# Optimization experiments

Measured on AMD Instinct MI355X. Metric: run time of the kernel, lower is better.

The kernel has to match this reference:

```python
import jax, jax.numpy as jnp
import numpy as np

DIM = 768
NH = 12
HD = DIM // NH
MLP = 4 * DIM
EPS = 1e-5


def _ln(x, w, b):
    mu = x.mean(-1, keepdims=True)
    var = ((x - mu) ** 2).mean(-1, keepdims=True)
    return (x - mu) * jax.lax.rsqrt(var + EPS) * w + b


def setup_inputs() -> dict:
    key = jax.random.key(0)
    ks = jax.random.split(key, 12)
    s = 0.02
    return {
        "xq": jax.random.normal(ks[0], (4, 32, 32, DIM), jnp.float32),
        "xkv": jax.random.normal(ks[1], (4, 64, 64, DIM), jnp.float32),
        "norm1_w": jnp.ones((DIM,), jnp.float32),
        "norm1_b": jnp.zeros((DIM,), jnp.float32),
        "kv_w": jax.random.normal(ks[2], (DIM, 2 * DIM), jnp.float32) * s,
        "kv_b": jnp.zeros((2 * DIM,), jnp.float32),
        "q_w": jax.random.normal(ks[3], (DIM, DIM), jnp.float32) * s,
        "q_b": jnp.zeros((DIM,), jnp.float32),
        "proj_w": jax.random.normal(ks[4], (DIM, DIM), jnp.float32) * s,
        "proj_b": jnp.zeros((DIM,), jnp.float32),
        "norm2_w": jnp.ones((DIM,), jnp.float32),
        "norm2_b": jnp.zeros((DIM,), jnp.float32),
        "mlp_w1": jax.random.normal(ks[5], (DIM, MLP), jnp.float32) * s,
        "mlp_b1": jnp.zeros((MLP,), jnp.float32),
        "mlp_w2": jax.random.normal(ks[6], (MLP, DIM), jnp.float32) * s,
        "mlp_b2": jnp.zeros((DIM,), jnp.float32),
    }


def reference(xq, xkv, norm1_w, norm1_b, kv_w, kv_b, q_w, q_b, proj_w, proj_b,
              norm2_w, norm2_b, mlp_w1, mlp_b1, mlp_w2, mlp_b2):
    B, Hq, Wq, C = xq.shape
    _, H, W, _ = xkv.shape
    shortcut = xq
    xn = _ln(xq, norm1_w, norm1_b)
    # kv projection: [B, H*W, 2, NH, HD]
    kv = (xkv.reshape(B, H * W, C) @ kv_w + kv_b).reshape(B, H * W, 2, NH, HD)
    k = kv[:, :, 0].transpose(0, 2, 1, 3)  # [B, NH, HW, HD]
    v = kv[:, :, 1].transpose(0, 2, 1, 3)
    q = (xn.reshape(B, Hq * Wq, C) @ q_w + q_b).reshape(B, Hq * Wq, NH, HD).transpose(0, 2, 1, 3)
    scale = HD ** -0.5
    attn = jnp.einsum('bhqd,bhkd->bhqk', q * scale, k)
    attn = jax.nn.softmax(attn, axis=-1)
    o = jnp.einsum('bhqk,bhkd->bhqd', attn, v)  # [B, NH, HqWq, HD]
    o = o.transpose(0, 2, 1, 3).reshape(B, Hq, Wq, C)
    o = o @ proj_w + proj_b
    x = shortcut + o
    xn2 = _ln(x, norm2_w, norm2_b)
    mlp = jax.nn.gelu(xn2 @ mlp_w1 + mlp_b1, approximate=False) @ mlp_w2 + mlp_b2
    return x + mlp
```

## Files before the change

### kernel.cpp

```cpp
#include <hip/hip_runtime.h>
#include <hip/hip_bf16.h>
#include <math.h>

#define DIM 768
#define NH 12
#define HD 64
#define NQ 1024
#define NKV 4096
#define QSCALE 0.18033688011112042f

typedef __attribute__((ext_vector_type(4))) float f32x4;
typedef __attribute__((ext_vector_type(16))) float f32x16;
typedef __attribute__((ext_vector_type(8))) __bf16 bf16x8;
typedef __attribute__((ext_vector_type(8))) unsigned short u16x8;
typedef __attribute__((ext_vector_type(4))) unsigned short u16x4;
typedef unsigned short u16;

typedef const __attribute__((address_space(1))) void* gas_t;
typedef __attribute__((address_space(3))) void* las_t;

__device__ __forceinline__ void gl16(const void* g, void* l) {
    __builtin_amdgcn_global_load_lds((gas_t)g, (las_t)l, 16, 0, 0);
}

__device__ __forceinline__ u16 f2b(float x) {
    __bf16 h = (__bf16)x;
    return __builtin_bit_cast(u16, h);
}

__device__ __forceinline__ float b2f(u16 x) {
    unsigned int u = ((unsigned int)x) << 16;
    return __builtin_bit_cast(float, u);
}

__device__ __forceinline__ f32x4 mfma16(const u16* a, const u16* b, f32x4 c) {
    bf16x8 av = *reinterpret_cast<const bf16x8*>(a);
    bf16x8 bv = *reinterpret_cast<const bf16x8*>(b);
    return __builtin_amdgcn_mfma_f32_16x16x32_bf16(av, bv, c, 0, 0, 0);
}

__device__ __forceinline__ f32x16 mfma32(bf16x8 a, bf16x8 b, f32x16 c) {
    return __builtin_amdgcn_mfma_f32_32x32x16_bf16(a, b, c, 0, 0, 0);
}

__global__ __launch_bounds__(256) void cast_bf16_kernel(
    const float* __restrict__ in, u16* __restrict__ out, int n8)
{
    int i = blockIdx.x * 256 + threadIdx.x;
    if (i >= n8) return;
    const float4* p = reinterpret_cast<const float4*>(in) + (size_t)i * 2;
    float4 a = p[0], b = p[1];
    u16x8 o;
    o[0] = f2b(a.x); o[1] = f2b(a.y); o[2] = f2b(a.z); o[3] = f2b(a.w);
    o[4] = f2b(b.x); o[5] = f2b(b.y); o[6] = f2b(b.z); o[7] = f2b(b.w);
    reinterpret_cast<u16x8*>(out)[i] = o;
}

__global__ __launch_bounds__(256) void transpose_cast_kernel(
    const float* __restrict__ W, u16* __restrict__ Wt, int K, int N)
{
    __shared__ u16 T[64][72];
    int k0 = blockIdx.y * 64, n0 = blockIdx.x * 64;
    int tid = threadIdx.x;
    int r = tid >> 2, c = (tid & 3) * 16;
    const float* src = W + (size_t)(k0 + r) * N + n0 + c;
    #pragma unroll
    for (int j = 0; j < 16; j += 4) {
        float4 f = *reinterpret_cast<const float4*>(src + j);
        T[r][c + j + 0] = f2b(f.x); T[r][c + j + 1] = f2b(f.y);
        T[r][c + j + 2] = f2b(f.z); T[r][c + j + 3] = f2b(f.w);
    }
    __syncthreads();
    int d = tid >> 2, c2 = (tid & 3) * 16;
    u16x8 o0, o1;
    #pragma unroll
    for (int j = 0; j < 8; ++j) o0[j] = T[c2 + j][d];
    #pragma unroll
    for (int j = 0; j < 8; ++j) o1[j] = T[c2 + 8 + j][d];
    u16* dst = Wt + (size_t)(n0 + d) * K + k0 + c2;
    *reinterpret_cast<u16x8*>(dst) = o0;
    *reinterpret_cast<u16x8*>(dst + 8) = o1;
}

__global__ __launch_bounds__(256) void ln_kernel(
    const float* __restrict__ x, const float* __restrict__ w,
    const float* __restrict__ b, u16* __restrict__ out)
{
    int row = blockIdx.x;
    const float* xr = x + (size_t)row * DIM;
    int tid = threadIdx.x;
    float v0 = xr[tid], v1 = xr[tid + 256], v2 = xr[tid + 512];
    float s = v0 + v1 + v2;
    float s2 = v0 * v0 + v1 * v1 + v2 * v2;
    for (int off = 1; off < 64; off <<= 1) {
        s += __shfl_xor(s, off);
        s2 += __shfl_xor(s2, off);
    }
    __shared__ float ss[4], ss2[4];
    int wid = tid >> 6, lane = tid & 63;
    if (lane == 0) { ss[wid] = s; ss2[wid] = s2; }
    __syncthreads();
    s = ss[0] + ss[1] + ss[2] + ss[3];
    s2 = ss2[0] + ss2[1] + ss2[2] + ss2[3];
    float mu = s * (1.0f / DIM);
    float var = s2 * (1.0f / DIM) - mu * mu;
    float r = rsqrtf(var + 1e-5f);
    u16* orow = out + (size_t)row * DIM;
    orow[tid]       = f2b((v0 - mu) * r * w[tid]       + b[tid]);
    orow[tid + 256] = f2b((v1 - mu) * r * w[tid + 256] + b[tid + 256]);
    orow[tid + 512] = f2b((v2 - mu) * r * w[tid + 512] + b[tid + 512]);
}

template <int EPI>
__global__ __launch_bounds__(256) void gemm_kernel(
    const u16* __restrict__ A, const u16* __restrict__ Bt,
    const float* __restrict__ bias, const float* __restrict__ res,
    void* __restrict__ out, void* __restrict__ out2, int M, int N, int K)
{
    __shared__ u16 As[2][4096];
    __shared__ u16 Bs[2][4096];
    int p = blockIdx.x;
    int nbx = N >> 7;
    int ypx = (M >> 7) >> 3;
    int xcd = p & 7, slot = p >> 3;
    int by = xcd * ypx + slot / nbx;
    int bx = slot - (slot / nbx) * nbx;
    int n0 = bx * 128, m0 = by * 128;
    int tid = threadIdx.x, lane = tid & 63, wave = tid >> 6;
    int wm = (wave >> 1) * 64, wn = (wave & 1) * 64;
    f32x4 acc[4][4] = {};

    int ca = tid, cb = tid + 256;
    int ra = ca >> 2, sa = ((ca & 3) ^ (ra & 3)) * 8;
    int rb = cb >> 2, sb = ((cb & 3) ^ (rb & 3)) * 8;
    const u16* Asrc1 = A + (size_t)(m0 + ra) * K + sa;
    const u16* Asrc2 = A + (size_t)(m0 + rb) * K + sb;
    const u16* Bsrc1 = Bt + (size_t)(n0 + ra) * K + sa;
    const u16* Bsrc2 = Bt + (size_t)(n0 + rb) * K + sb;

    auto STAGE = [&](int buf, int k0) {
        gl16(Asrc1 + k0, &As[buf][ca * 8]);
        gl16(Asrc2 + k0, &As[buf][cb * 8]);
        gl16(Bsrc1 + k0, &Bs[buf][ca * 8]);
        gl16(Bsrc2 + k0, &Bs[buf][cb * 8]);
    };

    int fr = lane & 15, fq = lane >> 4;
    int co = (fq ^ (fr & 3)) * 8;

    auto COMPUTE = [&](int buf) {
        #pragma unroll
        for (int mf = 0; mf < 4; ++mf) {
            const u16* a = &As[buf][(wm + mf * 16 + fr) * 32 + co];
            #pragma unroll
            for (int nf = 0; nf < 4; ++nf)
                acc[mf][nf] = mfma16(a, &Bs[buf][(wn + nf * 16 + fr) * 32 + co],
                                     acc[mf][nf]);
        }
    };

    STAGE(0, 0);
    asm volatile("s_waitcnt vmcnt(0)" ::: "memory");
    __builtin_amdgcn_s_barrier();
    for (int k0 = 0; k0 < K; k0 += 64) {
        STAGE(1, k0 + 32);
        COMPUTE(0);
        asm volatile("s_waitcnt vmcnt(0)" ::: "memory");
        __builtin_amdgcn_s_barrier();
        if (k0 + 64 < K) STAGE(0, k0 + 64);
        COMPUTE(1);
        asm volatile("s_waitcnt vmcnt(0)" ::: "memory");
        __builtin_amdgcn_s_barrier();
    }

    if constexpr (EPI == 4) {
        u16* kb = reinterpret_cast<u16*>(out);
        u16* vtb = reinterpret_cast<u16*>(out2);
        if (n0 < 768) {
            #pragma unroll
            for (int mf = 0; mf < 4; ++mf)
                #pragma unroll
                for (int nf = 0; nf < 4; ++nf) {
                    int col = n0 + wn + nf * 16 + fr;
                    float bv = bias[col];
                    #pragma unroll
                    for (int r = 0; r < 4; ++r) {
                        int row = m0 + wm + mf * 16 + fq * 4 + r;
                        kb[(size_t)row * 768 + col] = f2b(acc[mf][nf][r] + bv);
                    }
                }
        } else {
            #pragma unroll
            for (int mf = 0; mf < 4; ++mf)
                #pragma unroll
                for (int nf = 0; nf < 4; ++nf) {
                    int col = n0 + wn + nf * 16 + fr;
                    int c = col - 768, h = c >> 6, d = c & 63;
                    float bv = bias[col];
                    int row0 = m0 + wm + mf * 16 + fq * 4;
                    int bb = row0 >> 12, kvi = row0 & 4095;
                    int kv6 = kvi & 63;
                    int slot = (kv6 & 51) | ((kv6 & 4) << 1) | ((kv6 & 8) >> 1);
                    u16x4 pv;
                    #pragma unroll
                    for (int r = 0; r < 4; ++r) pv[r] = f2b(acc[mf][nf][r] + bv);
                    *reinterpret_cast<u16x4*>(vtb + ((size_t)(bb * 12 + h) * 64 + d) * 4096
                                              + (kvi & ~63) + slot) = pv;
                }
        }
        return;
    }

    float* outf = reinterpret_cast<float*>(out);
    u16* outb = reinterpret_cast<u16*>(out);
    #pragma unroll
    for (int mf = 0; mf < 4; ++mf)
        #pragma unroll
        for (int nf = 0; nf < 4; ++nf)
            #pragma unroll
            for (int r = 0; r < 4; ++r) {
                int row = m0 + wm + mf * 16 + fq * 4 + r;
                int col = n0 + wn + nf * 16 + fr;
                size_t idx = (size_t)row * N + col;
                float v = acc[mf][nf][r] + bias[col];
                if constexpr (EPI == 2) {
                    outf[idx] = v + res[idx];
                } else {
                    float g = 0.5f * v * (1.0f + erff(v * 0.70710678118f));
                    outb[idx] = f2b(g);
                }
            }
}

template <int EPI>
__global__ __launch_bounds__(256) void gemm64_kernel(
    const u16* __restrict__ A, const u16* __restrict__ Bt,
    const float* __restrict__ bias, const float* __restrict__ res,
    void* __restrict__ out, int M, int N, int K)
{
    __shared__ u16 As[2][4096];
    __shared__ u16 Bs[2][4096];
    int p = blockIdx.x;
    int nbx = N >> 6;
    int ypx = (M >> 6) >> 3;
    int xcd = p & 7, slot = p >> 3;
    int by = xcd * ypx + slot / nbx;
    int bx = slot - (slot / nbx) * nbx;
    int n0 = bx * 64, m0 = by * 64;
    int tid = threadIdx.x, lane = tid & 63, wave = tid >> 6;
    int wm = (wave >> 1) * 32, wn = (wave & 1) * 32;
    f32x4 acc[2][2] = {};

    int c1 = tid, c2 = tid + 256;
    int r1 = c1 >> 3, s1 = ((c1 & 7) ^ (r1 & 7)) * 8;
    int r2 = c2 >> 3, s2 = ((c2 & 7) ^ (r2 & 7)) * 8;
    const u16* As1 = A + (size_t)(m0 + r1) * K + s1;
    const u16* As2 = A + (size_t)(m0 + r2) * K + s2;
    const u16* Bt1 = Bt + (size_t)(n0 + r1) * K + s1;
    const u16* Bt2 = Bt + (size_t)(n0 + r2) * K + s2;

    auto STAGE = [&](int buf, int k0) {
        gl16(As1 + k0, &As[buf][c1 * 8]);
        gl16(As2 + k0, &As[buf][c2 * 8]);
        gl16(Bt1 + k0, &Bs[buf][c1 * 8]);
        gl16(Bt2 + k0, &Bs[buf][c2 * 8]);
    };

    int fr = lane & 15, fq = lane >> 4;
    int co0 = (fq ^ (fr & 7)) * 8;
    int co1 = ((4 + fq) ^ (fr & 7)) * 8;

    STAGE(0, 0);
    asm volatile("s_waitcnt vmcnt(0)" ::: "memory");
    __builtin_amdgcn_s_barrier();
    int NIT = K >> 6;
    for (int it = 0; it < NIT; ++it) {
        int cur = it & 1;
        if (it + 1 < NIT) STAGE(cur ^ 1, (it + 1) << 6);
        #pragma unroll
        for (int mf = 0; mf < 2; ++mf) {
            const u16* arow = &As[cur][(wm + mf * 16 + fr) * 64];
            #pragma unroll
            for (int nf = 0; nf < 2; ++nf) {
                const u16* brow = &Bs[cur][(wn + nf * 16 + fr) * 64];
                acc[mf][nf] = mfma16(arow + co0, brow + co0, acc[mf][nf]);
                acc[mf][nf] = mfma16(arow + co1, brow + co1, acc[mf][nf]);
            }
        }
        asm volatile("s_waitcnt vmcnt(0)" ::: "memory");
        __builtin_amdgcn_s_barrier();
    }

    float* outf = reinterpret_cast<float*>(out);
    u16* outb = reinterpret_cast<u16*>(out);
    #pragma unroll
    for (int mf = 0; mf < 2; ++mf)
        #pragma unroll
        for (int nf = 0; nf < 2; ++nf)
            #pragma unroll
            for (int r = 0; r < 4; ++r) {
                int row = m0 + wm + mf * 16 + fq * 4 + r;
                int col = n0 + wn + nf * 16 + fr;
                size_t idx = (size_t)row * N + col;
                float v = acc[mf][nf][r] + bias[col];
                if constexpr (EPI == 1) {
                    outb[idx] = f2b(v * QSCALE);
                } else {
                    outf[idx] = v + res[idx];
                }
            }
}

__global__ __launch_bounds__(256, 4) void attn_kernel(
    const u16* __restrict__ q, const u16* __restrict__ kbuf,
    const u16* __restrict__ vt, u16* __restrict__ op0, u16* __restrict__ op1,
    float* __restrict__ L)
{
    int p = blockIdx.x;
    int xcd = p & 7, slot = p >> 3;
    int bh = xcd * 6 + (slot >> 5);
    int rem = slot & 31;
    int qt = rem >> 1, half = rem & 1;
    int h = bh % NH, bb = bh / NH;
    const int NIT = 32;

    __shared__ u16 Kb[2][4096];
    __shared__ u16 Vb[2][4096];
    __shared__ float lx[64];

    int tid = threadIdx.x, lane = tid & 63, wave = tid >> 6;
    int qb = wave >> 1, kh = wave & 1;
    int l31 = lane & 31, hi = lane >> 5;
    int sw = l31 & 7;

    u16x8 ov = {0x3F80, 0x3F80, 0x3F80, 0x3F80, 0x3F80, 0x3F80, 0x3F80, 0x3F80};
    const bf16x8 ONES = __builtin_bit_cast(bf16x8, ov);

    bf16x8 qf[4];
    {
        const u16* qbp = q + (size_t)(bb * NQ + qt * 64 + qb * 32 + l31) * DIM
                         + h * HD + hi * 8;
        #pragma unroll
        for (int ks = 0; ks < 4; ++ks)
            qf[ks] = *reinterpret_cast<const bf16x8*>(qbp + ks * 16);
    }

    int c1 = tid, c2 = tid + 256;
    int r1 = c1 >> 3, sc1 = (c1 & 7) ^ (r1 & 7);
    int r2 = c2 >> 3, sc2 = (c2 & 7) ^ (r2 & 7);
    size_t krow0 = (size_t)bb * NKV + half * 2048;
    const u16* ks1 = kbuf + (krow0 + r1) * 768 + h * HD + sc1 * 8;
    const u16* ks2 = kbuf + (krow0 + r2) * 768 + h * HD + sc2 * 8;
    const u16* vs1 = vt + ((size_t)bh * HD + r1) * NKV + half * 2048 + sc1 * 8;
    const u16* vs2 = vt + ((size_t)bh * HD + r2) * NKV + half * 2048 + sc2 * 8;

    auto STAGE = [&](int buf, int kv0) {
        gl16(ks1 + (size_t)kv0 * 768, &Kb[buf][c1 * 8]);
        gl16(ks2 + (size_t)kv0 * 768, &Kb[buf][c2 * 8]);
        gl16(vs1 + kv0, &Vb[buf][c1 * 8]);
        gl16(vs2 + kv0, &Vb[buf][c2 * 8]);
    };

    f32x16 oacc0 = {}, oacc1 = {}, lsum = {};

    STAGE(0, 0);
    asm volatile("s_waitcnt vmcnt(0)" ::: "memory");
    __builtin_amdgcn_s_barrier();

    int krow = kh * 32 + l31;
    const int kroff = krow * 64;
    int vc0 = ((kh * 4 + 0 * 2 + hi) ^ sw) * 8;
    int vc1 = ((kh * 4 + 1 * 2 + hi) ^ sw) * 8;
    int krsw = krow & 7;

    auto BODY = [&](int cur, int it) {
        if (it + 1 < NIT) STAGE(cur ^ 1, (it + 1) * 64);
        const u16* kb = &Kb[cur][kroff];
        const u16* vb = &Vb[cur][l31 * 64];
        f32x16 s = {};
        __builtin_amdgcn_s_setprio(1);
        #pragma unroll
        for (int ks = 0; ks < 4; ++ks) {
            bf16x8 kf = *reinterpret_cast<const bf16x8*>(
                kb + (((ks * 2 + hi) ^ krsw) * 8));
            s = mfma32(kf, qf[ks], s);
        }
        __builtin_amdgcn_s_setprio(0);
        u16x8 p0, p1;
        #pragma unroll
        for (int r = 0; r < 8; ++r) p0[r] = f2b(exp2f(s[r]));
        #pragma unroll
        for (int r = 0; r < 8; ++r) p1[r] = f2b(exp2f(s[r + 8]));
        bf16x8 a0 = __builtin_bit_cast(bf16x8, p0);
        bf16x8 a1 = __builtin_bit_cast(bf16x8, p1);
        __builtin_amdgcn_s_setprio(1);
        lsum = mfma32(a0, ONES, lsum);
        lsum = mfma32(a1, ONES, lsum);
        bf16x8 v00 = *reinterpret_cast<const bf16x8*>(vb + vc0);
        bf16x8 v01 = *reinterpret_cast<const bf16x8*>(vb + vc1);
        bf16x8 v10 = *reinterpret_cast<const bf16x8*>(vb + 2048 + vc0);
        bf16x8 v11 = *reinterpret_cast<const bf16x8*>(vb + 2048 + vc1);
        oacc0 = mfma32(a0, v00, oacc0);
        oacc0 = mfma32(a1, v01, oacc0);
        oacc1 = mfma32(a0, v10, oacc1);
        oacc1 = mfma32(a1, v11, oacc1);
        __builtin_amdgcn_s_setprio(0);
        asm volatile("s_waitcnt vmcnt(0)" ::: "memory");
        __builtin_amdgcn_s_barrier();
    };

    for (int it = 0; it < NIT; it += 2) { BODY(0, it); BODY(1, it + 1); }

    float* ox = reinterpret_cast<float*>(&Kb[0][0]);
    if (kh) {
        #pragma unroll
        for (int r = 0; r < 16; ++r) {
            int qrow = (r & 3) + 8 * (r >> 2) + 4 * hi;
            ox[(qb * 32 + qrow) * 64 + l31] = oacc0[r];
            ox[(qb * 32 + qrow) * 64 + 32 + l31] = oacc1[r];
        }
        if (l31 == 0) {
            #pragma unroll
            for (int r = 0; r < 16; ++r) {
                int qrow = (r & 3) + 8 * (r >> 2) + 4 * hi;
                lx[qb * 32 + qrow] = lsum[r];
            }
        }
    }
    __syncthreads();
    if (!kh) {
        u16* op = half ? op1 : op0;
        float lt[16];
        #pragma unroll
        for (int r = 0; r < 16; ++r) {
            int qrow = (r & 3) + 8 * (r >> 2) + 4 * hi;
            lt[r] = lsum[r] + lx[qb * 32 + qrow];
        }
        if (l31 == 0) {
            #pragma unroll
            for (int r = 0; r < 16; ++r) {
                int qrow = (r & 3) + 8 * (r >> 2) + 4 * hi;
                L[half * 49152 + bh * 1024 + qt * 64 + qb * 32 + qrow] = lt[r];
            }
        }
        #pragma unroll
        for (int r = 0; r < 16; ++r) {
            int qrow = (r & 3) + 8 * (r >> 2) + 4 * hi;
            float rcl = 1.0f / lt[r];
            float t0 = oacc0[r] + ox[(qb * 32 + qrow) * 64 + l31];
            float t1 = oacc1[r] + ox[(qb * 32 + qrow) * 64 + 32 + l31];
            size_t orow = (size_t)(bb * NQ + qt * 64 + qb * 32 + qrow) * DIM + h * HD;
            op[orow + l31] = f2b(t0 * rcl);
            op[orow + 32 + l31] = f2b(t1 * rcl);
        }
    }
}

__global__ __launch_bounds__(256) void combine_kernel(
    const u16* __restrict__ op0, const u16* __restrict__ op1,
    const float* __restrict__ L, u16* __restrict__ out)
{
    int idx = blockIdx.x * 256 + threadIdx.x;
    int t = idx / 96, cc = (idx - t * 96) * 8;
    int h = cc >> 6;
    int bb = t >> 10, qr = t & 1023;
    int li = (bb * 12 + h) * 1024 + qr;
    float l0 = L[li], l1 = L[49152 + li];
    float w0 = l0 / (l0 + l1), w1 = 1.0f - w0;
    u16x8 a = *reinterpret_cast<const u16x8*>(op0 + (size_t)t * 768 + cc);
    u16x8 b = *reinterpret_cast<const u16x8*>(op1 + (size_t)t * 768 + cc);
    u16x8 o;
    #pragma unroll
    for (int j = 0; j < 8; ++j) o[j] = f2b(b2f(a[j]) * w0 + b2f(b[j]) * w1);
    *reinterpret_cast<u16x8*>(out + (size_t)t * 768 + cc) = o;
}

extern "C" void kernel_launch(void* const* d_in, const int* in_sizes, int n_in,
                              void* d_out, int out_size, void* d_ws, size_t ws_size,
                              hipStream_t stream) {
    const float* xq  = (const float*)d_in[0];
    const float* xkv = (const float*)d_in[1];
    const float* n1w = (const float*)d_in[2];
    const float* n1b = (const float*)d_in[3];
    const float* kvw = (const float*)d_in[4];
    const float* kvb = (const float*)d_in[5];
    const float* qw  = (const float*)d_in[6];
    const float* qb  = (const float*)d_in[7];
    const float* pjw = (const float*)d_in[8];
    const float* pjb = (const float*)d_in[9];
    const float* n2w = (const float*)d_in[10];
    const float* n2b = (const float*)d_in[11];
    const float* w1  = (const float*)d_in[12];
    const float* b1  = (const float*)d_in[13];
    const float* w2  = (const float*)d_in[14];
    const float* b2  = (const float*)d_in[15];
    float* xout = (float*)d_out;

    char* ws = (char*)d_ws;
    u16* xkv_b  = (u16*)(ws);
    u16* kbuf   = (u16*)(ws + 25165824);
    u16* vt     = (u16*)(ws + 50331648);
    u16* xn_bf  = (u16*)(ws + 75497472);
    u16* q_bf   = (u16*)(ws + 81788928);
    u16* o_bf   = (u16*)(ws + 88080384);
    u16* wkv_bf = (u16*)(ws + 94371840);
    u16* wq_bf  = (u16*)(ws + 96731136);
    u16* wpj_bf = (u16*)(ws + 97910784);
    u16* w1_bf  = (u16*)(ws + 99090432);
    u16* w2_bf  = (u16*)(ws + 103809024);
    u16* hid    = xkv_b;
    float* Lbuf = (float*)wkv_bf;

    cast_bf16_kernel<<<dim3(6144), dim3(256), 0, stream>>>(xkv, xkv_b, 1572864);
    transpose_cast_kernel<<<dim3(24, 12), dim3(256), 0, stream>>>(kvw, wkv_bf, 768, 1536);
    transpose_cast_kernel<<<dim3(12, 12), dim3(256), 0, stream>>>(qw, wq_bf, 768, 768);
    transpose_cast_kernel<<<dim3(12, 12), dim3(256), 0, stream>>>(pjw, wpj_bf, 768, 768);
    transpose_cast_kernel<<<dim3(48, 12), dim3(256), 0, stream>>>(w1, w1_bf, 768, 3072);
    transpose_cast_kernel<<<dim3(12, 48), dim3(256), 0, stream>>>(w2, w2_bf, 3072, 768);

    ln_kernel<<<dim3(4096), dim3(256), 0, stream>>>(xq, n1w, n1b, xn_bf);
    gemm_kernel<4><<<dim3(12 * 128), dim3(256), 0, stream>>>(xkv_b, wkv_bf, kvb, nullptr, kbuf, vt, 16384, 1536, 768);
    gemm64_kernel<1><<<dim3(768), dim3(256), 0, stream>>>(xn_bf, wq_bf, qb, nullptr, q_bf, 4096, 768, 768);
    attn_kernel<<<dim3(1536), dim3(256), 0, stream>>>(q_bf, kbuf, vt, xn_bf, o_bf, Lbuf);
    combine_kernel<<<dim3(1536), dim3(256), 0, stream>>>(xn_bf, o_bf, Lbuf, q_bf);
    gemm64_kernel<2><<<dim3(768), dim3(256), 0, stream>>>(q_bf, wpj_bf, pjb, xq, xout, 4096, 768, 768);
    ln_kernel<<<dim3(4096), dim3(256), 0, stream>>>(xout, n2w, n2b, xn_bf);
    gemm_kernel<3><<<dim3(24 * 32), dim3(256), 0, stream>>>(xn_bf, w1_bf, b1, nullptr, hid, nullptr, 4096, 3072, 768);
    gemm64_kernel<2><<<dim3(768), dim3(256), 0, stream>>>(hid, w2_bf, b2, xout, xout, 4096, 768, 3072);
}
```

Baseline: 290.9 us.

## Split attention KV into quarters with 128-query tiles, dropping intra-block reduction

Each attention block now handles 128 queries (one 32-row query slab per wave) over a quarter of the KV sequence, with each wave iterating over both 32-key halves of every staged tile. Previously a block covered 64 queries over half the KV, and two waves per query slab split the keys, so their partial outputs had to be merged through LDS with a barrier. That LDS merge disappears and each staged K/V tile is reused by twice as many queries. The cost is four partial outputs instead of two, so the combine kernel reads and weights four bf16 buffers and L values, which adds global memory traffic.

```diff
diff --git a/kernel.cpp b/kernel.cpp
--- a/kernel.cpp
+++ b/kernel.cpp
@@ -314,22 +314,20 @@
 __global__ __launch_bounds__(256, 4) void attn_kernel(
     const u16* __restrict__ q, const u16* __restrict__ kbuf,
     const u16* __restrict__ vt, u16* __restrict__ op0, u16* __restrict__ op1,
-    float* __restrict__ L)
+    u16* __restrict__ op2, u16* __restrict__ op3, float* __restrict__ L)
 {
     int p = blockIdx.x;
     int xcd = p & 7, slot = p >> 3;
     int bh = xcd * 6 + (slot >> 5);
     int rem = slot & 31;
-    int qt = rem >> 1, half = rem & 1;
+    int qt = rem >> 2, quarter = rem & 3;
     int h = bh % NH, bb = bh / NH;
-    const int NIT = 32;
+    const int NIT = 16;
 
     __shared__ u16 Kb[2][4096];
     __shared__ u16 Vb[2][4096];
-    __shared__ float lx[64];
 
     int tid = threadIdx.x, lane = tid & 63, wave = tid >> 6;
-    int qb = wave >> 1, kh = wave & 1;
     int l31 = lane & 31, hi = lane >> 5;
     int sw = l31 & 7;
 
@@ -338,7 +336,7 @@
 
     bf16x8 qf[4];
     {
-        const u16* qbp = q + (size_t)(bb * NQ + qt * 64 + qb * 32 + l31) * DIM
+        const u16* qbp = q + (size_t)(bb * NQ + qt * 128 + wave * 32 + l31) * DIM
                          + h * HD + hi * 8;
         #pragma unroll
         for (int ks = 0; ks < 4; ++ks)
@@ -348,11 +346,11 @@
     int c1 = tid, c2 = tid + 256;
     int r1 = c1 >> 3, sc1 = (c1 & 7) ^ (r1 & 7);
     int r2 = c2 >> 3, sc2 = (c2 & 7) ^ (r2 & 7);
-    size_t krow0 = (size_t)bb * NKV + half * 2048;
+    size_t krow0 = (size_t)bb * NKV + quarter * 1024;
     const u16* ks1 = kbuf + (krow0 + r1) * 768 + h * HD + sc1 * 8;
     const u16* ks2 = kbuf + (krow0 + r2) * 768 + h * HD + sc2 * 8;
-    const u16* vs1 = vt + ((size_t)bh * HD + r1) * NKV + half * 2048 + sc1 * 8;
-    const u16* vs2 = vt + ((size_t)bh * HD + r2) * NKV + half * 2048 + sc2 * 8;
+    const u16* vs1 = vt + ((size_t)bh * HD + r1) * NKV + quarter * 1024 + sc1 * 8;
+    const u16* vs2 = vt + ((size_t)bh * HD + r2) * NKV + quarter * 1024 + sc2 * 8;
 
     auto STAGE = [&](int buf, int kv0) {
         gl16(ks1 + (size_t)kv0 * 768, &Kb[buf][c1 * 8]);
@@ -367,97 +365,70 @@
     asm volatile("s_waitcnt vmcnt(0)" ::: "memory");
     __builtin_amdgcn_s_barrier();
 
-    int krow = kh * 32 + l31;
-    const int kroff = krow * 64;
-    int vc0 = ((kh * 4 + 0 * 2 + hi) ^ sw) * 8;
-    int vc1 = ((kh * 4 + 1 * 2 + hi) ^ sw) * 8;
-    int krsw = krow & 7;
-
     auto BODY = [&](int cur, int it) {
         if (it + 1 < NIT) STAGE(cur ^ 1, (it + 1) * 64);
-        const u16* kb = &Kb[cur][kroff];
         const u16* vb = &Vb[cur][l31 * 64];
-        f32x16 s = {};
-        __builtin_amdgcn_s_setprio(1);
-        #pragma unroll
-        for (int ks = 0; ks < 4; ++ks) {
-            bf16x8 kf = *reinterpret_cast<const bf16x8*>(
-                kb + (((ks * 2 + hi) ^ krsw) * 8));
-            s = mfma32(kf, qf[ks], s);
+        #pragma unroll
+        for (int kh = 0; kh < 2; ++kh) {
+            const u16* kb = &Kb[cur][(kh * 32 + l31) * 64];
+            f32x16 s = {};
+            __builtin_amdgcn_s_setprio(1);
+            #pragma unroll
+            for (int ks = 0; ks < 4; ++ks) {
+                bf16x8 kf = *reinterpret_cast<const bf16x8*>(
+                    kb + (((ks * 2 + hi) ^ sw) * 8));
+                s = mfma32(kf, qf[ks], s);
+            }
+            __builtin_amdgcn_s_setprio(0);
+            u16x8 p0, p1;
+            #pragma unroll
+            for (int r = 0; r < 8; ++r) p0[r] = f2b(exp2f(s[r]));
+            #pragma unroll
+            for (int r = 0; r < 8; ++r) p1[r] = f2b(exp2f(s[r + 8]));
+            bf16x8 a0 = __builtin_bit_cast(bf16x8, p0);
+            bf16x8 a1 = __builtin_bit_cast(bf16x8, p1);
+            int vc0 = ((kh * 4 + 0 + hi) ^ sw) * 8;
+            int vc1 = ((kh * 4 + 2 + hi) ^ sw) * 8;
+            __builtin_amdgcn_s_setprio(1);
+            lsum = mfma32(a0, ONES, lsum);
+            lsum = mfma32(a1, ONES, lsum);
+            bf16x8 v00 = *reinterpret_cast<const bf16x8*>(vb + vc0);
+            bf16x8 v01 = *reinterpret_cast<const bf16x8*>(vb + vc1);
+            bf16x8 v10 = *reinterpret_cast<const bf16x8*>(vb + 2048 + vc0);
+            bf16x8 v11 = *reinterpret_cast<const bf16x8*>(vb + 2048 + vc1);
+            oacc0 = mfma32(a0, v00, oacc0);
+            oacc0 = mfma32(a1, v01, oacc0);
+            oacc1 = mfma32(a0, v10, oacc1);
+            oacc1 = mfma32(a1, v11, oacc1);
+            __builtin_amdgcn_s_setprio(0);
         }
-        __builtin_amdgcn_s_setprio(0);
-        u16x8 p0, p1;
-        #pragma unroll
-        for (int r = 0; r < 8; ++r) p0[r] = f2b(exp2f(s[r]));
-        #pragma unroll
-        for (int r = 0; r < 8; ++r) p1[r] = f2b(exp2f(s[r + 8]));
-        bf16x8 a0 = __builtin_bit_cast(bf16x8, p0);
-        bf16x8 a1 = __builtin_bit_cast(bf16x8, p1);
-        __builtin_amdgcn_s_setprio(1);
-        lsum = mfma32(a0, ONES, lsum);
-        lsum = mfma32(a1, ONES, lsum);
-        bf16x8 v00 = *reinterpret_cast<const bf16x8*>(vb + vc0);
-        bf16x8 v01 = *reinterpret_cast<const bf16x8*>(vb + vc1);
-        bf16x8 v10 = *reinterpret_cast<const bf16x8*>(vb + 2048 + vc0);
-        bf16x8 v11 = *reinterpret_cast<const bf16x8*>(vb + 2048 + vc1);
-        oacc0 = mfma32(a0, v00, oacc0);
-        oacc0 = mfma32(a1, v01, oacc0);
-        oacc1 = mfma32(a0, v10, oacc1);
-        oacc1 = mfma32(a1, v11, oacc1);
-        __builtin_amdgcn_s_setprio(0);
         asm volatile("s_waitcnt vmcnt(0)" ::: "memory");
         __builtin_amdgcn_s_barrier();
     };
 
     for (int it = 0; it < NIT; it += 2) { BODY(0, it); BODY(1, it + 1); }
 
-    float* ox = reinterpret_cast<float*>(&Kb[0][0]);
-    if (kh) {
+    u16* op = (quarter == 0) ? op0 : (quarter == 1) ? op1 : (quarter == 2) ? op2 : op3;
+    #pragma unroll
+    for (int r = 0; r < 16; ++r) {
+        int qrow = (r & 3) + 8 * (r >> 2) + 4 * hi;
+        float rcl = 1.0f / lsum[r];
+        size_t orow = (size_t)(bb * NQ + qt * 128 + wave * 32 + qrow) * DIM + h * HD;
+        op[orow + l31] = f2b(oacc0[r] * rcl);
+        op[orow + 32 + l31] = f2b(oacc1[r] * rcl);
+    }
+    if (l31 == 0) {
         #pragma unroll
         for (int r = 0; r < 16; ++r) {
             int qrow = (r & 3) + 8 * (r >> 2) + 4 * hi;
-            ox[(qb * 32 + qrow) * 64 + l31] = oacc0[r];
-            ox[(qb * 32 + qrow) * 64 + 32 + l31] = oacc1[r];
-        }
-        if (l31 == 0) {
-            #pragma unroll
-            for (int r = 0; r < 16; ++r) {
-                int qrow = (r & 3) + 8 * (r >> 2) + 4 * hi;
-                lx[qb * 32 + qrow] = lsum[r];
-            }
-        }
-    }
-    __syncthreads();
-    if (!kh) {
-        u16* op = half ? op1 : op0;
-        float lt[16];
-        #pragma unroll
-        for (int r = 0; r < 16; ++r) {
-            int qrow = (r & 3) + 8 * (r >> 2) + 4 * hi;
-            lt[r] = lsum[r] + lx[qb * 32 + qrow];
-        }
-        if (l31 == 0) {
-            #pragma unroll
-            for (int r = 0; r < 16; ++r) {
-                int qrow = (r & 3) + 8 * (r >> 2) + 4 * hi;
-                L[half * 49152 + bh * 1024 + qt * 64 + qb * 32 + qrow] = lt[r];
-            }
-        }
-        #pragma unroll
-        for (int r = 0; r < 16; ++r) {
-            int qrow = (r & 3) + 8 * (r >> 2) + 4 * hi;
-            float rcl = 1.0f / lt[r];
-            float t0 = oacc0[r] + ox[(qb * 32 + qrow) * 64 + l31];
-            float t1 = oacc1[r] + ox[(qb * 32 + qrow) * 64 + 32 + l31];
-            size_t orow = (size_t)(bb * NQ + qt * 64 + qb * 32 + qrow) * DIM + h * HD;
-            op[orow + l31] = f2b(t0 * rcl);
-            op[orow + 32 + l31] = f2b(t1 * rcl);
+            L[quarter * 49152 + bh * 1024 + qt * 128 + wave * 32 + qrow] = lsum[r];
         }
     }
 }
 
 __global__ __launch_bounds__(256) void combine_kernel(
     const u16* __restrict__ op0, const u16* __restrict__ op1,
+    const u16* __restrict__ op2, const u16* __restrict__ op3,
     const float* __restrict__ L, u16* __restrict__ out)
 {
     int idx = blockIdx.x * 256 + threadIdx.x;
@@ -465,13 +436,16 @@
     int h = cc >> 6;
     int bb = t >> 10, qr = t & 1023;
     int li = (bb * 12 + h) * 1024 + qr;
-    float l0 = L[li], l1 = L[49152 + li];
-    float w0 = l0 / (l0 + l1), w1 = 1.0f - w0;
+    float l0 = L[li], l1 = L[49152 + li], l2 = L[2 * 49152 + li], l3 = L[3 * 49152 + li];
+    float rs = 1.0f / (l0 + l1 + l2 + l3);
     u16x8 a = *reinterpret_cast<const u16x8*>(op0 + (size_t)t * 768 + cc);
     u16x8 b = *reinterpret_cast<const u16x8*>(op1 + (size_t)t * 768 + cc);
+    u16x8 c = *reinterpret_cast<const u16x8*>(op2 + (size_t)t * 768 + cc);
+    u16x8 d = *reinterpret_cast<const u16x8*>(op3 + (size_t)t * 768 + cc);
     u16x8 o;
     #pragma unroll
-    for (int j = 0; j < 8; ++j) o[j] = f2b(b2f(a[j]) * w0 + b2f(b[j]) * w1);
+    for (int j = 0; j < 8; ++j)
+        o[j] = f2b((b2f(a[j]) * l0 + b2f(b[j]) * l1 + b2f(c[j]) * l2 + b2f(d[j]) * l3) * rs);
     *reinterpret_cast<u16x8*>(out + (size_t)t * 768 + cc) = o;
 }
 
@@ -509,6 +483,8 @@
     u16* w1_bf  = (u16*)(ws + 99090432);
     u16* w2_bf  = (u16*)(ws + 103809024);
     u16* hid    = xkv_b;
+    u16* op2    = xkv_b;
+    u16* op3    = (u16*)(ws + 6291456);
     float* Lbuf = (float*)wkv_bf;
 
     cast_bf16_kernel<<<dim3(6144), dim3(256), 0, stream>>>(xkv, xkv_b, 1572864);
@@ -521,8 +497,8 @@
     ln_kernel<<<dim3(4096), dim3(256), 0, stream>>>(xq, n1w, n1b, xn_bf);
     gemm_kernel<4><<<dim3(12 * 128), dim3(256), 0, stream>>>(xkv_b, wkv_bf, kvb, nullptr, kbuf, vt, 16384, 1536, 768);
     gemm64_kernel<1><<<dim3(768), dim3(256), 0, stream>>>(xn_bf, wq_bf, qb, nullptr, q_bf, 4096, 768, 768);
-    attn_kernel<<<dim3(1536), dim3(256), 0, stream>>>(q_bf, kbuf, vt, xn_bf, o_bf, Lbuf);
-    combine_kernel<<<dim3(1536), dim3(256), 0, stream>>>(xn_bf, o_bf, Lbuf, q_bf);
+    attn_kernel<<<dim3(1536), dim3(256), 0, stream>>>(q_bf, kbuf, vt, xn_bf, o_bf, op2, op3, Lbuf);
+    combine_kernel<<<dim3(1536), dim3(256), 0, stream>>>(xn_bf, o_bf, op2, op3, Lbuf, q_bf);
     gemm64_kernel<2><<<dim3(768), dim3(256), 0, stream>>>(q_bf, wpj_bf, pjb, xq, xout, 4096, 768, 768);
     ln_kernel<<<dim3(4096), dim3(256), 0, stream>>>(xout, n2w, n2b, xn_bf);
     gemm_kernel<3><<<dim3(24 * 32), dim3(256), 0, stream>>>(xn_bf, w1_bf, b1, nullptr, hid, nullptr, 4096, 3072, 768);
```

Result: no change. 286.2 us (-1.6%).
